# Kernel tuning notes

Measured on AMD Instinct MI355X. Metric: run time of the kernel, lower is better.

## Reference

```python
import jax, jax.numpy as jnp
from jax import lax
import numpy as np

IN_C, OUT_C, K, N_SPLIT = 256, 256, 3, 4
N_LEGO = int(OUT_C * 0.25)          # 64
BASIC_C = IN_C // N_SPLIT           # 64


def setup_inputs() -> dict:
    key = jax.random.key(0)
    k1, k2, k3, k4 = jax.random.split(key, 4)
    x = jax.random.normal(k1, (32, IN_C, 56, 56), dtype=jnp.float32)
    # kaiming-normal-ish initialization of parameters
    lego = jax.random.normal(k2, (N_LEGO, BASIC_C, K, 1), dtype=jnp.float32) * np.sqrt(2.0 / (BASIC_C * K))
    aux_coefficients = jax.random.normal(k3, (N_SPLIT, OUT_C, N_LEGO, 1, 1), dtype=jnp.float32) * np.sqrt(2.0 / N_LEGO)
    aux_combination = jax.random.normal(k4, (N_SPLIT, OUT_C, N_LEGO, 1, 1), dtype=jnp.float32) * np.sqrt(2.0 / N_LEGO)
    return {"x": x, "lego": lego, "aux_coefficients": aux_coefficients, "aux_combination": aux_combination}


def reference(x, lego, aux_coefficients, aux_combination):
    n_split, out_c, n_lego = aux_combination.shape[:3]
    bc = lego.shape[1]
    # one-hot selection: each (split, out_channel) picks exactly one lego feature
    idx = jnp.argmax(aux_combination[..., 0, 0], axis=2)              # (n_split, out_c)
    proxy = jax.nn.one_hot(idx, n_lego, dtype=x.dtype)                # (n_split, out_c, n_lego)
    W = aux_coefficients[..., 0, 0] * proxy                           # (n_split, out_c, n_lego)
    out = 0.0
    for i in range(n_split):
        xi = x[:, i * bc:(i + 1) * bc]                                # (B, bc, H, W)
        feat = lax.conv_general_dilated(
            xi, lego, window_strides=(3, 1), padding=((1, 1), (1, 1)),
            dimension_numbers=("NCHW", "OIHW", "NCHW"))               # (B, n_lego, Ho, Wo)
        out = out + jnp.einsum("bnhw,on->bohw", feat, W[i])
    return out
```

## Files before the change

kernel.cpp:

```cpp
#include <hip/hip_runtime.h>

#define INC    256
#define HIN    56
#define WIN    56
#define HOUT   19
#define WOUT   58
#define HW     3136

typedef short frag8 __attribute__((ext_vector_type(8)));
typedef float f32x4 __attribute__((ext_vector_type(4)));

static __device__ __forceinline__ unsigned short f2bf(float f) {
    unsigned u = __float_as_uint(f);
    u += 0x7fffu + ((u >> 16) & 1u);
    return (unsigned short)(u >> 16);
}

static __device__ __forceinline__ unsigned cvtpk(float a, float b) {
    unsigned r;
    asm("v_cvt_pk_bf16_f32 %0, %1, %2" : "=v"(r) : "v"(a), "v"(b));
    return r;
}

#define VMCNT(n) asm volatile("s_waitcnt vmcnt(" #n ")" ::: "memory")
#define LGKM0()  asm volatile("s_waitcnt lgkmcnt(0)" ::: "memory")
#define FENCE()  asm volatile("" ::: "memory")
#define SB0()    __builtin_amdgcn_sched_barrier(0)

__global__ __launch_bounds__(256) void prep_weff(
    const float* __restrict__ lego,
    const float* __restrict__ coefs,
    const float* __restrict__ comb,
    unsigned short* __restrict__ Asw)
{
    __shared__ int   idxS[4];
    __shared__ float cofS[4];
    const int t  = threadIdx.x;
    const int kx = blockIdx.x;
    const int o  = blockIdx.y;
    const int wv = t >> 6, l = t & 63;

    float v  = comb[(wv * 256 + o) * 64 + l];
    int   bi = l;
    #pragma unroll
    for (int off = 32; off >= 1; off >>= 1) {
        float ov = __shfl_xor(v, off, 64);
        int   oi = __shfl_xor(bi, off, 64);
        if (ov > v || (ov == v && oi < bi)) { v = ov; bi = oi; }
    }
    if (l == 0) {
        idxS[wv] = bi;
        cofS[wv] = coefs[(wv * 256 + o) * 64 + bi];
    }
    __syncthreads();

    const int k  = kx * 256 + t;
    const int kh = k >> 8, c = k & 255;
    const int i  = c >> 6, cl = c & 63;
    float w = cofS[i] * lego[idxS[i] * 192 + cl * 3 + kh];

    const int o_tile = o >> 4, m = o & 15;
    const int ks = k >> 5, kc = (k >> 3) & 3, j = k & 7;
    const int ks2 = ks >> 1, ksl = ks & 1;
    Asw[((((size_t)ks2 * 16 + o_tile) * 2 + ksl) * 64 + kc * 16 + m) * 8 + j] = f2bf(w);
}

__global__ __launch_bounds__(256, 3) void conv_mfma(
    const float* __restrict__ x,
    const unsigned short* __restrict__ Asw,
    float* __restrict__ out)
{
    __shared__ unsigned short Xs[2][4096];

    const int t  = threadIdx.x;
    const int h  = blockIdx.x;
    const int b  = blockIdx.y;
    const int l  = t & 63;
    const int lo = l & 15;
    const int hi = l >> 4;
    const int wv = t >> 6;

    const int cw   = t & 31;
    const int kg   = (t >> 5) & 7;
    const int kslw = kg >> 2, kcw = kg & 3;
    const int c1u  = cw + 32;
    const int c1   = (c1u < WIN) ? c1u : (WIN - 1);
    int voff[16];
    #pragma unroll
    for (int j = 0; j < 8; ++j) {
        voff[j]     = (kg * 8 + j) * HW + cw;
        voff[8 + j] = (kg * 8 + j) * HW + c1;
    }
    const int ws0 = (kslw * 4 + (cw  >> 4)) * 64 + kcw * 16 + (cw  & 15);
    const int ws1 = (kslw * 4 + (c1u >> 4)) * 64 + kcw * 16 + (c1u & 15);
    unsigned short* Wp[2][2];
    Wp[0][0] = &Xs[0][ws0 * 8];  Wp[0][1] = &Xs[0][ws1 * 8];
    Wp[1][0] = &Xs[1][ws0 * 8];  Wp[1][1] = &Xs[1][ws1 * 8];

    const float* xb = x + (size_t)b * (INC * HW);
    const frag8* Afw = (const frag8*)Asw + l;
    const frag8* Xf[2] = { (const frag8*)&Xs[0][0] + l,
                           (const frag8*)&Xs[1][0] + l };

    f32x4 acc[4][4];
    #pragma unroll
    for (int ot = 0; ot < 4; ++ot)
        #pragma unroll
        for (int wt = 0; wt < 4; ++wt)
            acc[ot][wt] = (f32x4){0.f, 0.f, 0.f, 0.f};

    frag8 A[4][2];
    float Lv[16];

    auto LOADL = [&](int q) {
        const int kh  = q >> 2, cq = q & 3;
        const int row = 3 * h - 1 + kh;
        const int rc  = row < 0 ? 0 : row;
        const float zmask = row < 0 ? 0.f : 1.f;
        const float* xq = xb + (size_t)cq * 64 * HW + (size_t)rc * WIN;
        #pragma unroll
        for (int i = 0; i < 16; ++i) Lv[i] = xq[voff[i]] * zmask;
    };

    auto LOADA = [&](int q) {
        #pragma unroll
        for (int ot = 0; ot < 4; ++ot)
            #pragma unroll
            for (int ksl = 0; ksl < 2; ++ksl)
                A[ot][ksl] = Afw[q * 2048 + wv * 512 + ot * 128 + ksl * 64];
    };

    auto W = [&](int q) {
        const int bp = q & 1;
        union { frag8 fr; unsigned u[4]; } P;
        P.u[0] = cvtpk(Lv[0], Lv[1]);
        P.u[1] = cvtpk(Lv[2], Lv[3]);
        P.u[2] = cvtpk(Lv[4], Lv[5]);
        P.u[3] = cvtpk(Lv[6], Lv[7]);
        *(frag8*)Wp[bp][0] = P.fr;
        P.u[0] = cvtpk(Lv[8],  Lv[9]);
        P.u[1] = cvtpk(Lv[10], Lv[11]);
        P.u[2] = cvtpk(Lv[12], Lv[13]);
        P.u[3] = cvtpk(Lv[14], Lv[15]);
        *(frag8*)Wp[bp][1] = P.fr;
    };

    LOADA(0);
    SB0();
    LOADL(0);
    SB0();
    VMCNT(0);
    W(0);
    LOADL(1);
    SB0();
    LGKM0();
    __builtin_amdgcn_s_barrier();
    FENCE();

    #pragma unroll
    for (int q = 0; q < 12; ++q) {
        const int bp = q & 1;
        #pragma unroll
        for (int ksl = 0; ksl < 2; ++ksl) {
            #pragma unroll
            for (int wt = 0; wt < 4; ++wt) {
                frag8 B = Xf[bp][(ksl * 4 + wt) * 64];
                #pragma unroll
                for (int ot = 0; ot < 4; ++ot)
                    acc[ot][wt] = __builtin_amdgcn_mfma_f32_16x16x32_bf16(
                        A[ot][ksl], B, acc[ot][wt], 0, 0, 0);
            }
        }

        if (q < 11) {
            SB0();
            LOADA(q + 1);
            SB0();
            VMCNT(8);
            W(q + 1);
            if (q < 10) LOADL(q + 2);
            SB0();
            LGKM0();
            __builtin_amdgcn_s_barrier();
            FENCE();
        }
    }

    #pragma unroll
    for (int ot = 0; ot < 4; ++ot) {
        #pragma unroll
        for (int r = 0; r < 4; ++r) {
            int o = wv * 64 + ot * 16 + hi * 4 + r;
            float* orow = out + ((size_t)(b * 256 + o) * HOUT + h) * WOUT;
            #pragma unroll
            for (int wt = 0; wt < 4; ++wt) {
                int n = wt * 16 + lo;
                if (n < 56) orow[n + 1] = acc[ot][wt][r];
            }
            if (lo == 0) orow[0]  = 0.f;
            if (lo == 1) orow[57] = 0.f;
        }
    }
}

extern "C" void kernel_launch(void* const* d_in, const int* in_sizes, int n_in,
                              void* d_out, int out_size, void* d_ws, size_t ws_size,
                              hipStream_t stream) {
    const float* x     = (const float*)d_in[0];
    const float* lego  = (const float*)d_in[1];
    const float* coefs = (const float*)d_in[2];
    const float* comb  = (const float*)d_in[3];
    float* out = (float*)d_out;

    unsigned short* Asw = (unsigned short*)d_ws;

    prep_weff<<<dim3(3, 256), 256, 0, stream>>>(lego, coefs, comb, Asw);
    conv_mfma<<<dim3(HOUT, 32), 256, 0, stream>>>(x, Asw, out);
}
```

Baseline: 197.0 us.

## Process two batch images per block to reuse weight fragments, rotate channel order

Each block now handles two batch images (b and b+16) for the same output row, so every A-weight fragment loaded from global is reused across twice as many MFMAs, and the grid is halved. It also rotates the channel-quarter iteration order per block to spread concurrent reads across different x slices. In exchange, accumulator registers and LDS per block double and the launch bound drops to 2 blocks per CU, which lowers occupancy and latency hiding. The VMCNT(8) wait is left unchanged even though each stage now issues twice as many global loads.

```diff
diff --git a/kernel.cpp b/kernel.cpp
--- a/kernel.cpp
+++ b/kernel.cpp
@@ -65,93 +65,116 @@
     Asw[((((size_t)ks2 * 16 + o_tile) * 2 + ksl) * 64 + kc * 16 + m) * 8 + j] = f2bf(w);
 }
 
-__global__ __launch_bounds__(256, 3) void conv_mfma(
+__global__ __launch_bounds__(256, 2) void conv_mfma(
     const float* __restrict__ x,
     const unsigned short* __restrict__ Asw,
     float* __restrict__ out)
 {
-    __shared__ unsigned short Xs[2][4096];
+    __shared__ unsigned short Xs[2][2][4096];
 
     const int t  = threadIdx.x;
     const int h  = blockIdx.x;
-    const int b  = blockIdx.y;
+    const int by = blockIdx.y;
+    const int bA = by, bB = by + 16;
     const int l  = t & 63;
     const int lo = l & 15;
     const int hi = l >> 4;
     const int wv = t >> 6;
+
+    const int lin = by * 19 + h;
+    const int rot = (lin >> 3) & 3;
 
     const int cw   = t & 31;
     const int kg   = (t >> 5) & 7;
     const int kslw = kg >> 2, kcw = kg & 3;
     const int c1u  = cw + 32;
     const int c1   = (c1u < WIN) ? c1u : (WIN - 1);
-    int voff[16];
-    #pragma unroll
-    for (int j = 0; j < 8; ++j) {
-        voff[j]     = (kg * 8 + j) * HW + cw;
-        voff[8 + j] = (kg * 8 + j) * HW + c1;
-    }
-    const int ws0 = (kslw * 4 + (cw  >> 4)) * 64 + kcw * 16 + (cw  & 15);
-    const int ws1 = (kslw * 4 + (c1u >> 4)) * 64 + kcw * 16 + (c1u & 15);
-    unsigned short* Wp[2][2];
-    Wp[0][0] = &Xs[0][ws0 * 8];  Wp[0][1] = &Xs[0][ws1 * 8];
-    Wp[1][0] = &Xs[1][ws0 * 8];  Wp[1][1] = &Xs[1][ws1 * 8];
-
-    const float* xb = x + (size_t)b * (INC * HW);
+    const int cdelta = c1 - cw;
+    int voff[8];
+    #pragma unroll
+    for (int j = 0; j < 8; ++j) voff[j] = (kg * 8 + j) * HW + cw;
+    const int ws0 = ((kslw * 4 + (cw  >> 4)) * 64 + kcw * 16 + (cw  & 15)) * 8;
+    const int ws1 = ((kslw * 4 + (c1u >> 4)) * 64 + kcw * 16 + (c1u & 15)) * 8;
+
+    const float* xbA = x + (size_t)bA * (INC * HW);
+    const float* xbB = x + (size_t)bB * (INC * HW);
     const frag8* Afw = (const frag8*)Asw + l;
-    const frag8* Xf[2] = { (const frag8*)&Xs[0][0] + l,
-                           (const frag8*)&Xs[1][0] + l };
-
-    f32x4 acc[4][4];
+
+    f32x4 accA[4][4], accB[4][4];
     #pragma unroll
     for (int ot = 0; ot < 4; ++ot)
         #pragma unroll
-        for (int wt = 0; wt < 4; ++wt)
-            acc[ot][wt] = (f32x4){0.f, 0.f, 0.f, 0.f};
+        for (int wt = 0; wt < 4; ++wt) {
+            accA[ot][wt] = (f32x4){0.f, 0.f, 0.f, 0.f};
+            accB[ot][wt] = (f32x4){0.f, 0.f, 0.f, 0.f};
+        }
 
     frag8 A[4][2];
-    float Lv[16];
-
-    auto LOADL = [&](int q) {
-        const int kh  = q >> 2, cq = q & 3;
-        const int row = 3 * h - 1 + kh;
-        const int rc  = row < 0 ? 0 : row;
-        const float zmask = row < 0 ? 0.f : 1.f;
-        const float* xq = xb + (size_t)cq * 64 * HW + (size_t)rc * WIN;
-        #pragma unroll
-        for (int i = 0; i < 16; ++i) Lv[i] = xq[voff[i]] * zmask;
-    };
-
-    auto LOADA = [&](int q) {
-        #pragma unroll
-        for (int ot = 0; ot < 4; ++ot)
-            #pragma unroll
-            for (int ksl = 0; ksl < 2; ++ksl)
-                A[ot][ksl] = Afw[q * 2048 + wv * 512 + ot * 128 + ksl * 64];
-    };
-
-    auto W = [&](int q) {
-        const int bp = q & 1;
-        union { frag8 fr; unsigned u[4]; } P;
-        P.u[0] = cvtpk(Lv[0], Lv[1]);
-        P.u[1] = cvtpk(Lv[2], Lv[3]);
-        P.u[2] = cvtpk(Lv[4], Lv[5]);
-        P.u[3] = cvtpk(Lv[6], Lv[7]);
-        *(frag8*)Wp[bp][0] = P.fr;
-        P.u[0] = cvtpk(Lv[8],  Lv[9]);
-        P.u[1] = cvtpk(Lv[10], Lv[11]);
-        P.u[2] = cvtpk(Lv[12], Lv[13]);
-        P.u[3] = cvtpk(Lv[14], Lv[15]);
-        *(frag8*)Wp[bp][1] = P.fr;
-    };
-
-    LOADA(0);
+    float LvA[16], LvB[16];
+
+#define QE(qv) (((qv) & 12) | (((qv) + rot) & 3))
+
+#define LOADL_T(LV, XB, QEV) do {                                          \
+        const int qe_ = (QEV);                                             \
+        const int row_ = 3 * h - 1 + (qe_ >> 2);                           \
+        const int rc_  = row_ < 0 ? 0 : row_;                              \
+        const float zm_ = row_ < 0 ? 0.f : 1.f;                            \
+        const float* xq_ = (XB) + (size_t)(qe_ & 3) * 64 * HW              \
+                                + (size_t)rc_ * WIN;                       \
+        _Pragma("unroll")                                                  \
+        for (int j_ = 0; j_ < 8; ++j_) {                                   \
+            LV[j_]     = xq_[voff[j_]] * zm_;                              \
+            LV[8 + j_] = xq_[voff[j_] + cdelta] * zm_;                     \
+        }                                                                  \
+    } while (0)
+
+#define LOADA_T(QEV) do {                                                  \
+        const int qe_ = (QEV);                                             \
+        _Pragma("unroll")                                                  \
+        for (int ot_ = 0; ot_ < 4; ++ot_)                                  \
+            _Pragma("unroll")                                              \
+            for (int ksl_ = 0; ksl_ < 2; ++ksl_)                           \
+                A[ot_][ksl_] = Afw[qe_ * 2048 + wv * 512 + ot_ * 128 + ksl_ * 64]; \
+    } while (0)
+
+#define W_T(BP, TL, LV) do {                                               \
+        union { frag8 fr; unsigned u[4]; } P_;                             \
+        P_.u[0] = cvtpk(LV[0], LV[1]);                                     \
+        P_.u[1] = cvtpk(LV[2], LV[3]);                                     \
+        P_.u[2] = cvtpk(LV[4], LV[5]);                                     \
+        P_.u[3] = cvtpk(LV[6], LV[7]);                                     \
+        *(frag8*)&Xs[BP][TL][ws0] = P_.fr;                                 \
+        P_.u[0] = cvtpk(LV[8],  LV[9]);                                    \
+        P_.u[1] = cvtpk(LV[10], LV[11]);                                   \
+        P_.u[2] = cvtpk(LV[12], LV[13]);                                   \
+        P_.u[3] = cvtpk(LV[14], LV[15]);                                   \
+        *(frag8*)&Xs[BP][TL][ws1] = P_.fr;                                 \
+    } while (0)
+
+#define COMPUTE_T(BP, TL, ACC) do {                                        \
+        const frag8* Xf_ = (const frag8*)&Xs[BP][TL][0] + l;               \
+        _Pragma("unroll")                                                  \
+        for (int ksl_ = 0; ksl_ < 2; ++ksl_)                               \
+            _Pragma("unroll")                                              \
+            for (int wt_ = 0; wt_ < 4; ++wt_) {                            \
+                frag8 B_ = Xf_[(ksl_ * 4 + wt_) * 64];                     \
+                _Pragma("unroll")                                          \
+                for (int ot_ = 0; ot_ < 4; ++ot_)                          \
+                    ACC[ot_][wt_] = __builtin_amdgcn_mfma_f32_16x16x32_bf16( \
+                        A[ot_][ksl_], B_, ACC[ot_][wt_], 0, 0, 0);         \
+            }                                                              \
+    } while (0)
+
+    LOADA_T(QE(0));
     SB0();
-    LOADL(0);
+    LOADL_T(LvA, xbA, QE(0));
+    LOADL_T(LvB, xbB, QE(0));
     SB0();
     VMCNT(0);
-    W(0);
-    LOADL(1);
+    W_T(0, 0, LvA);
+    W_T(0, 1, LvB);
+    LOADL_T(LvA, xbA, QE(1));
+    LOADL_T(LvB, xbB, QE(1));
     SB0();
     LGKM0();
     __builtin_amdgcn_s_barrier();
@@ -160,25 +183,20 @@
     #pragma unroll
     for (int q = 0; q < 12; ++q) {
         const int bp = q & 1;
-        #pragma unroll
-        for (int ksl = 0; ksl < 2; ++ksl) {
-            #pragma unroll
-            for (int wt = 0; wt < 4; ++wt) {
-                frag8 B = Xf[bp][(ksl * 4 + wt) * 64];
-                #pragma unroll
-                for (int ot = 0; ot < 4; ++ot)
-                    acc[ot][wt] = __builtin_amdgcn_mfma_f32_16x16x32_bf16(
-                        A[ot][ksl], B, acc[ot][wt], 0, 0, 0);
-            }
-        }
+        COMPUTE_T(bp, 0, accA);
+        COMPUTE_T(bp, 1, accB);
 
         if (q < 11) {
             SB0();
-            LOADA(q + 1);
+            LOADA_T(QE(q + 1));
             SB0();
             VMCNT(8);
-            W(q + 1);
-            if (q < 10) LOADL(q + 2);
+            W_T((q + 1) & 1, 0, LvA);
+            W_T((q + 1) & 1, 1, LvB);
+            if (q < 10) {
+                LOADL_T(LvA, xbA, QE(q + 2));
+                LOADL_T(LvB, xbB, QE(q + 2));
+            }
             SB0();
             LGKM0();
             __builtin_amdgcn_s_barrier();
@@ -186,21 +204,25 @@
         }
     }
 
-    #pragma unroll
-    for (int ot = 0; ot < 4; ++ot) {
-        #pragma unroll
-        for (int r = 0; r < 4; ++r) {
-            int o = wv * 64 + ot * 16 + hi * 4 + r;
-            float* orow = out + ((size_t)(b * 256 + o) * HOUT + h) * WOUT;
-            #pragma unroll
-            for (int wt = 0; wt < 4; ++wt) {
-                int n = wt * 16 + lo;
-                if (n < 56) orow[n + 1] = acc[ot][wt][r];
-            }
-            if (lo == 0) orow[0]  = 0.f;
-            if (lo == 1) orow[57] = 0.f;
-        }
-    }
+#define STORE_T(BV, ACC) do {                                              \
+        _Pragma("unroll")                                                  \
+        for (int ot_ = 0; ot_ < 4; ++ot_)                                  \
+            _Pragma("unroll")                                              \
+            for (int r_ = 0; r_ < 4; ++r_) {                               \
+                int o_ = wv * 64 + ot_ * 16 + hi * 4 + r_;                 \
+                float* orow_ = out + ((size_t)((BV) * 256 + o_) * HOUT + h) * WOUT; \
+                _Pragma("unroll")                                          \
+                for (int wt_ = 0; wt_ < 4; ++wt_) {                        \
+                    int n_ = wt_ * 16 + lo;                                \
+                    if (n_ < 56) orow_[n_ + 1] = ACC[ot_][wt_][r_];        \
+                }                                                          \
+                if (lo == 0) orow_[0]  = 0.f;                              \
+                if (lo == 1) orow_[57] = 0.f;                              \
+            }                                                              \
+    } while (0)
+
+    STORE_T(bA, accA);
+    STORE_T(bB, accB);
 }
 
 extern "C" void kernel_launch(void* const* d_in, const int* in_sizes, int n_in,
@@ -215,5 +237,5 @@
     unsigned short* Asw = (unsigned short*)d_ws;
 
     prep_weff<<<dim3(3, 256), 256, 0, stream>>>(lego, coefs, comb, Asw);
-    conv_mfma<<<dim3(HOUT, 32), 256, 0, stream>>>(x, Asw, out);
-}
+    conv_mfma<<<dim3(HOUT, 16), 256, 0, stream>>>(x, Asw, out);
+}
```

Result: slower. 247.7 us (+25.7%).

## Deepen conv pipeline to three register stages and four LDS buffers

Applied to the files above, without the earlier changes.

Restructures the MFMA conv main loop so global loads of x are issued three steps ahead into rotating register sets, and LDS is grown to four buffers. The write of the next tile to LDS is placed before the MFMAs on the current buffer. The aim is to hide global-load latency better and remove a wait between compute and LDS store. In exchange it uses more registers and LDS, so occupancy drops from 3 to 2 blocks per CU.

```diff
diff --git a/kernel.cpp b/kernel.cpp
--- a/kernel.cpp
+++ b/kernel.cpp
@@ -65,12 +65,12 @@
     Asw[((((size_t)ks2 * 16 + o_tile) * 2 + ksl) * 64 + kc * 16 + m) * 8 + j] = f2bf(w);
 }
 
-__global__ __launch_bounds__(256, 3) void conv_mfma(
+__global__ __launch_bounds__(256, 2) void conv_mfma(
     const float* __restrict__ x,
     const unsigned short* __restrict__ Asw,
     float* __restrict__ out)
 {
-    __shared__ unsigned short Xs[2][4096];
+    __shared__ unsigned short Xs[4][4096];
 
     const int t  = threadIdx.x;
     const int h  = blockIdx.x;
@@ -91,16 +91,11 @@
         voff[j]     = (kg * 8 + j) * HW + cw;
         voff[8 + j] = (kg * 8 + j) * HW + c1;
     }
-    const int ws0 = (kslw * 4 + (cw  >> 4)) * 64 + kcw * 16 + (cw  & 15);
-    const int ws1 = (kslw * 4 + (c1u >> 4)) * 64 + kcw * 16 + (c1u & 15);
-    unsigned short* Wp[2][2];
-    Wp[0][0] = &Xs[0][ws0 * 8];  Wp[0][1] = &Xs[0][ws1 * 8];
-    Wp[1][0] = &Xs[1][ws0 * 8];  Wp[1][1] = &Xs[1][ws1 * 8];
+    const int ws0 = ((kslw * 4 + (cw  >> 4)) * 64 + kcw * 16 + (cw  & 15)) * 8;
+    const int ws1 = ((kslw * 4 + (c1u >> 4)) * 64 + kcw * 16 + (c1u & 15)) * 8;
 
     const float* xb = x + (size_t)b * (INC * HW);
     const frag8* Afw = (const frag8*)Asw + l;
-    const frag8* Xf[2] = { (const frag8*)&Xs[0][0] + l,
-                           (const frag8*)&Xs[1][0] + l };
 
     f32x4 acc[4][4];
     #pragma unroll
@@ -110,9 +105,9 @@
             acc[ot][wt] = (f32x4){0.f, 0.f, 0.f, 0.f};
 
     frag8 A[4][2];
-    float Lv[16];
-
-    auto LOADL = [&](int q) {
+    float LvA[16], LvB[16], LvC[16];
+
+    auto LOADL = [&](float (&Lv)[16], int q) {
         const int kh  = q >> 2, cq = q & 3;
         const int row = 3 * h - 1 + kh;
         const int rc  = row < 0 ? 0 : row;
@@ -130,61 +125,94 @@
                 A[ot][ksl] = Afw[q * 2048 + wv * 512 + ot * 128 + ksl * 64];
     };
 
-    auto W = [&](int q) {
-        const int bp = q & 1;
+    auto W = [&](float (&Lv)[16], int buf) {
         union { frag8 fr; unsigned u[4]; } P;
         P.u[0] = cvtpk(Lv[0], Lv[1]);
         P.u[1] = cvtpk(Lv[2], Lv[3]);
         P.u[2] = cvtpk(Lv[4], Lv[5]);
         P.u[3] = cvtpk(Lv[6], Lv[7]);
-        *(frag8*)Wp[bp][0] = P.fr;
+        *(frag8*)&Xs[buf][ws0] = P.fr;
         P.u[0] = cvtpk(Lv[8],  Lv[9]);
         P.u[1] = cvtpk(Lv[10], Lv[11]);
         P.u[2] = cvtpk(Lv[12], Lv[13]);
         P.u[3] = cvtpk(Lv[14], Lv[15]);
-        *(frag8*)Wp[bp][1] = P.fr;
-    };
-
-    LOADA(0);
-    SB0();
-    LOADL(0);
-    SB0();
-    VMCNT(0);
-    W(0);
-    LOADL(1);
-    SB0();
-    LGKM0();
-    __builtin_amdgcn_s_barrier();
-    FENCE();
-
-    #pragma unroll
-    for (int q = 0; q < 12; ++q) {
-        const int bp = q & 1;
+        *(frag8*)&Xs[buf][ws1] = P.fr;
+    };
+
+    auto COMPUTE = [&](int buf) {
+        const frag8* Xf = (const frag8*)&Xs[buf][0] + l;
         #pragma unroll
         for (int ksl = 0; ksl < 2; ++ksl) {
             #pragma unroll
             for (int wt = 0; wt < 4; ++wt) {
-                frag8 B = Xf[bp][(ksl * 4 + wt) * 64];
+                frag8 B = Xf[(ksl * 4 + wt) * 64];
                 #pragma unroll
                 for (int ot = 0; ot < 4; ++ot)
                     acc[ot][wt] = __builtin_amdgcn_mfma_f32_16x16x32_bf16(
                         A[ot][ksl], B, acc[ot][wt], 0, 0, 0);
             }
         }
-
-        if (q < 11) {
-            SB0();
-            LOADA(q + 1);
-            SB0();
-            VMCNT(8);
-            W(q + 1);
-            if (q < 10) LOADL(q + 2);
-            SB0();
-            LGKM0();
-            __builtin_amdgcn_s_barrier();
-            FENCE();
-        }
-    }
+    };
+
+    LOADA(0);
+    SB0();
+    LOADL(LvA, 0);
+    LOADL(LvB, 1);
+    LOADL(LvC, 2);
+    SB0();
+    VMCNT(32);
+    W(LvA, 0);
+    SB0();
+    LGKM0();
+    __builtin_amdgcn_s_barrier();
+    FENCE();
+
+#define ROUND(q, SW, SL, VM)                                               \
+    do {                                                                   \
+        VM;                                                                \
+        W(SW, (q + 1) & 3);                                                \
+        COMPUTE(q & 3);                                                    \
+        SB0();                    \
+        LOADA(q + 1);             \
+        SB0();                                                             \
+        LOADL(SL, q + 3);                                                  \
+        SB0();                                                             \
+        LGKM0();                  \
+        __builtin_amdgcn_s_barrier();                                      \
+        FENCE();                                                           \
+    } while (0)
+
+    ROUND(0, LvB, LvA, VMCNT(16));
+    ROUND(1, LvC, LvB, VMCNT(24));
+    ROUND(2, LvA, LvC, VMCNT(24));
+    ROUND(3, LvB, LvA, VMCNT(24));
+    ROUND(4, LvC, LvB, VMCNT(24));
+    ROUND(5, LvA, LvC, VMCNT(24));
+    ROUND(6, LvB, LvA, VMCNT(24));
+    ROUND(7, LvC, LvB, VMCNT(24));
+    ROUND(8, LvA, LvC, VMCNT(24));
+
+    VMCNT(24);
+    W(LvB, 10 & 3);
+    COMPUTE(9 & 3);
+    SB0();
+    LOADA(10);
+    SB0();
+    LGKM0();
+    __builtin_amdgcn_s_barrier();
+    FENCE();
+
+    VMCNT(8);
+    W(LvC, 11 & 3);
+    COMPUTE(10 & 3);
+    SB0();
+    LOADA(11);
+    SB0();
+    LGKM0();
+    __builtin_amdgcn_s_barrier();
+    FENCE();
+
+    COMPUTE(11 & 3);
 
     #pragma unroll
     for (int ot = 0; ot < 4; ++ot) {
```

Result: no change. 195.0 us (-1.1%).
